# Optimization experiments

Hardware: AMD Instinct MI355X
Metric: run time of the kernel (lower is better)

The kernel has to match this reference:

```python
import jax, jax.numpy as jnp
import numpy as np

N, E, DIN, HID, HEADS = 50000, 400000, 256, 64, 4
EPS_BN = 1e-5

def setup_inputs() -> dict:
    key = jax.random.key(0)
    ks = jax.random.split(key, 12)
    inp = {}
    inp['x'] = jax.random.normal(ks[0], (N, DIN), dtype=jnp.float32)
    inp['edge_index'] = jax.random.randint(ks[1], (2, E), 0, N, dtype=jnp.int64)
    s = 1.0 / np.sqrt(DIN)
    inp['W1'] = jax.random.uniform(ks[2], (DIN, HEADS * HID), jnp.float32, -s, s)
    inp['a_src1'] = jax.random.normal(ks[3], (HEADS, HID), dtype=jnp.float32) * 0.1
    inp['a_dst1'] = jax.random.normal(ks[4], (HEADS, HID), dtype=jnp.float32) * 0.1
    inp['b1'] = jnp.zeros((HEADS * HID,), jnp.float32)
    inp['bn1_w'] = jnp.ones((HEADS * HID,), jnp.float32)
    inp['bn1_b'] = jnp.zeros((HEADS * HID,), jnp.float32)
    inp['bn1_m'] = jnp.zeros((HEADS * HID,), jnp.float32)
    inp['bn1_v'] = jnp.ones((HEADS * HID,), jnp.float32)
    s2 = 1.0 / np.sqrt(HEADS * HID)
    inp['W2'] = jax.random.uniform(ks[5], (HEADS * HID, HID), jnp.float32, -s2, s2)
    inp['a_src2'] = jax.random.normal(ks[6], (1, HID), dtype=jnp.float32) * 0.1
    inp['a_dst2'] = jax.random.normal(ks[7], (1, HID), dtype=jnp.float32) * 0.1
    inp['b2'] = jnp.zeros((HID,), jnp.float32)
    inp['bn2_w'] = jnp.ones((HID,), jnp.float32)
    inp['bn2_b'] = jnp.zeros((HID,), jnp.float32)
    inp['bn2_m'] = jnp.zeros((HID,), jnp.float32)
    inp['bn2_v'] = jnp.ones((HID,), jnp.float32)
    sr = 1.0 / np.sqrt(HID)
    inp['Wr'] = jax.random.uniform(ks[8], (HID, 1), jnp.float32, -sr, sr)
    inp['br'] = jnp.zeros((1,), jnp.float32)
    inp['Wc'] = jax.random.uniform(ks[9], (HID, 1), jnp.float32, -sr, sr)
    inp['bc'] = jnp.zeros((1,), jnp.float32)
    return inp

def gat_layer(x, src, dst, W, a_src, a_dst, bias, concat):
    # x: [N, Fin] -> h: [N, H, D]
    H, D = a_src.shape
    h = (x @ W).reshape(-1, H, D)
    alpha_s = jnp.sum(h * a_src[None], axis=-1)  # [N, H]
    alpha_d = jnp.sum(h * a_dst[None], axis=-1)
    e = jax.nn.leaky_relu(alpha_s[src] + alpha_d[dst], 0.2)  # [Et, H]
    m = jax.ops.segment_max(e, dst, num_segments=N)
    m = jnp.where(jnp.isfinite(m), m, 0.0)
    ex = jnp.exp(e - m[dst])
    denom = jax.ops.segment_sum(ex, dst, num_segments=N)
    alpha = ex / (denom[dst] + 1e-16)  # segment softmax over incoming edges
    msg = h[src] * alpha[:, :, None]  # [Et, H, D]
    out = jax.ops.segment_sum(msg, dst, num_segments=N)  # [N, H, D]
    out = out.reshape(N, H * D) if concat else out.mean(axis=1)
    return out + bias

def batchnorm(x, w, b, mean, var):
    return (x - mean) * jax.lax.rsqrt(var + EPS_BN) * w + b

def reference(x, edge_index, W1, a_src1, a_dst1, b1, bn1_w, bn1_b, bn1_m, bn1_v,
              W2, a_src2, a_dst2, b2, bn2_w, bn2_b, bn2_m, bn2_v, Wr, br, Wc, bc):
    # add self loops (PyG GATConv default)
    loops = jnp.arange(N, dtype=edge_index.dtype)
    src = jnp.concatenate([edge_index[0], loops])
    dst = jnp.concatenate([edge_index[1], loops])
    h = gat_layer(x, src, dst, W1, a_src1, a_dst1, b1, concat=True)
    h = jax.nn.elu(batchnorm(h, bn1_w, bn1_b, bn1_m, bn1_v))
    h = gat_layer(h, src, dst, W2, a_src2, a_dst2, b2, concat=False)
    h = jax.nn.elu(batchnorm(h, bn2_w, bn2_b, bn2_m, bn2_v))
    reg = h @ Wr + br
    clf = jax.nn.sigmoid(h @ Wc + bc)
    return reg, clf
```

## Files before the change

### kernel.cpp

```cpp
#include <hip/hip_runtime.h>
#include <math.h>


typedef unsigned short ushort_t;
typedef unsigned char uchar_t;
typedef __attribute__((ext_vector_type(8))) unsigned short ushort8;
typedef __attribute__((ext_vector_type(4))) unsigned short ushort4v;
typedef __attribute__((ext_vector_type(8))) short short8;
typedef __attribute__((ext_vector_type(4))) float f32x4;
typedef __attribute__((ext_vector_type(2))) float f32x2;

#define EPS_BN 1e-5f

__device__ __forceinline__ ushort_t f2bf(float f) {
  unsigned u = __float_as_uint(f);
  unsigned r = u + 0x7fffu + ((u >> 16) & 1u);
  return (ushort_t)(r >> 16);
}
__device__ __forceinline__ float bf2f(ushort_t h) {
  return __uint_as_float((unsigned)h << 16);
}
__device__ __forceinline__ uchar_t f2fp8(float f) {
  return (uchar_t)(__builtin_amdgcn_cvt_pk_fp8_f32(f, f, 0, false) & 0xff);
}
__device__ __forceinline__ float leaky02(float x) { return x >= 0.f ? x : 0.2f * x; }
__device__ __forceinline__ float elu_fast(float x) {
  return x > 0.f ? x : __expf(x) - 1.f;
}
__device__ __forceinline__ float wave_sum(float v) {
#pragma unroll
  for (int o = 1; o < 64; o <<= 1) v += __shfl_xor(v, o, 64);
  return v;
}
__device__ __forceinline__ int wave_incl_scan(int v, int lane) {
#pragma unroll
  for (int off = 1; off < 64; off <<= 1) {
    int t = __shfl_up(v, off, 64);
    if (lane >= off) v += t;
  }
  return v;
}

__device__ __forceinline__ void gld_lds16(const ushort_t* g, ushort_t* l) {
  __builtin_amdgcn_global_load_lds(
      (const __attribute__((address_space(1))) unsigned int*)g,
      (__attribute__((address_space(3))) unsigned int*)l, 16, 0, 0);
}

__global__ __launch_bounds__(256) void hist_kernel(
    const int* __restrict__ dst, int* __restrict__ counts, int E) {
  int e = blockIdx.x * blockDim.x + threadIdx.x;
  if (e < E) atomicAdd(&counts[dst[e]], 1);
}

__global__ __launch_bounds__(256) void scan_chunks_kernel(
    const int* __restrict__ counts, int* __restrict__ offsets, int* __restrict__ partials,
    int N, int E, int* __restrict__ csr_src,
    const float* __restrict__ W1, const float* __restrict__ W2,
    ushort_t* __restrict__ W1t, ushort_t* __restrict__ W2t,
    const float* __restrict__ b1, const float* __restrict__ bn1w,
    const float* __restrict__ bn1b, const float* __restrict__ bn1m,
    const float* __restrict__ bn1v,
    const float* __restrict__ b2, const float* __restrict__ bn2w,
    const float* __restrict__ bn2b, const float* __restrict__ bn2m,
    const float* __restrict__ bn2v,
    float* __restrict__ S1, float* __restrict__ T1,
    float* __restrict__ S2, float* __restrict__ T2) {
  __shared__ int ws[4];
  const int tid = threadIdx.x, lane = tid & 63, wv = tid >> 6;
  const int i = blockIdx.x * 256 + tid;
  const int gsz = gridDim.x * 256;
  int v = (i < N) ? counts[i] : 0;
  int incl = wave_incl_scan(v, lane);
  if (lane == 63) ws[wv] = incl;
  __syncthreads();
  int wbase = 0;
  for (int k = 0; k < wv; ++k) wbase += ws[k];
  if (i < N) offsets[i] = wbase + incl - v;
  if (tid == 255) partials[blockIdx.x] = wbase + incl;

  for (int j = i; j < 256 * 256; j += gsz) {
    int k = j >> 8, n2 = j & 255;
    W1t[n2 * 256 + k] = f2bf(W1[j]);
  }
  for (int j = i; j < 256 * 64; j += gsz) {
    int k = j >> 6, n2 = j & 63;
    W2t[n2 * 256 + k] = f2bf(W2[j]);
  }
  if (i < 256) {
    float s = bn1w[i] * rsqrtf(bn1v[i] + EPS_BN);
    S1[i] = s;
    T1[i] = (b1[i] - bn1m[i]) * s + bn1b[i];
  } else if (i < 320) {
    int j = i - 256;
    float s = bn2w[j] * rsqrtf(bn2v[j] + EPS_BN);
    S2[j] = s;
    T2[j] = (b2[j] - bn2m[j]) * s + bn2b[j];
  } else if (i < 384) {
    csr_src[E + i - 320] = 0;
  }
}

__global__ __launch_bounds__(256) void scatter_kernel(
    const int* __restrict__ src, const int* __restrict__ dst,
    const int* __restrict__ offsets, const int* __restrict__ partials,
    int* __restrict__ cursor, int* __restrict__ csr_src,
    int* __restrict__ offs2, int E, int N, int nb) {
  __shared__ int pp[256];
  __shared__ int ws[4];
  __shared__ int tot;
  const int tid = threadIdx.x, lane = tid & 63, wv = tid >> 6;
  int v = (tid < nb) ? partials[tid] : 0;
  int incl = wave_incl_scan(v, lane);
  if (lane == 63) ws[wv] = incl;
  __syncthreads();
  int wbase = 0;
  for (int k = 0; k < wv; ++k) wbase += ws[k];
  pp[tid] = wbase + incl - v;
  if (tid == 255) tot = wbase + incl;
  __syncthreads();

  int idx = blockIdx.x * 256 + tid;
  if (idx < E) {
    int d = dst[idx];
    int p = atomicAdd(&cursor[d], 1);
    csr_src[offsets[d] + pp[d >> 8] + p] = src[idx];
  }
  if (idx <= N) {
    offs2[idx] = (idx < N) ? offsets[idx] + pp[idx >> 8] : tot;
  }
}

__global__ __launch_bounds__(512) void gemm1_persist(
    const float* __restrict__ X, const ushort_t* __restrict__ Bt,
    uchar_t* __restrict__ Cout, const float* __restrict__ avs,
    const float* __restrict__ avd,
    float* __restrict__ as_out, float* __restrict__ ad_out, int M, int ntiles) {
  __shared__ ushort_t Bs[256 * 256];
  __shared__ ushort_t As[32 * 256];
  const int t = threadIdx.x;
  const int w = t >> 6, l = t & 63;
  const int wr = w >> 2, wc = w & 3;

#pragma unroll
  for (int it = 0; it < 16; ++it) {
    int s = it * 512 + t;
    int i = s >> 5, sr = s & 31;
    int kb = sr >> 3, sl8 = sr & 7;
    int kc = (sl8 ^ (i & 7)) << 3;
    gld_lds16(Bt + (size_t)i * 256 + kb * 64 + kc, &Bs[s * 8]);
  }

  const int ar = t >> 4, k0a = (t & 15) * 16;
  int wd0, wd1;
  {
    int k = k0a;
    wd0 = ar * 256 + (k & ~63) + ((k & 63) ^ ((ar & 7) << 3));
    k = k0a + 8;
    wd1 = ar * 256 + (k & ~63) + ((k & 63) ^ ((ar & 7) << 3));
  }
  float4 fa0, fa1, fa2, fa3;
  {
    const float* src = X + (size_t)min(blockIdx.x * 32 + ar, M - 1) * 256 + k0a;
    fa0 = *(const float4*)(src);
    fa1 = *(const float4*)(src + 4);
    fa2 = *(const float4*)(src + 8);
    fa3 = *(const float4*)(src + 12);
  }

  const int fr = l & 15;
  const int kq = (l >> 4) << 3;
  const int fx = (fr & 7) << 3;
  const ushort_t* Ab = &As[(wr * 16 + fr) << 8];
  const ushort_t* Bb = &Bs[(wc * 64 + fr) << 8];

  float asw[4], adw[4];
#pragma unroll
  for (int j = 0; j < 4; ++j) {
    asw[j] = avs[wc * 64 + fr + j * 16];
    adw[j] = avd[wc * 64 + fr + j * 16];
  }

  for (int tile = blockIdx.x; tile < ntiles; tile += 256) {
    ushort8 u0, u1;
    u0[0] = f2bf(fa0.x); u0[1] = f2bf(fa0.y); u0[2] = f2bf(fa0.z); u0[3] = f2bf(fa0.w);
    u0[4] = f2bf(fa1.x); u0[5] = f2bf(fa1.y); u0[6] = f2bf(fa1.z); u0[7] = f2bf(fa1.w);
    u1[0] = f2bf(fa2.x); u1[1] = f2bf(fa2.y); u1[2] = f2bf(fa2.z); u1[3] = f2bf(fa2.w);
    u1[4] = f2bf(fa3.x); u1[5] = f2bf(fa3.y); u1[6] = f2bf(fa3.z); u1[7] = f2bf(fa3.w);
    __syncthreads();
    *(ushort8*)&As[wd0] = u0;
    *(ushort8*)&As[wd1] = u1;
    __syncthreads();

    {
      int nt_ = tile + 256;
      if (nt_ < ntiles) {
        const float* src = X + (size_t)min(nt_ * 32 + ar, M - 1) * 256 + k0a;
        fa0 = *(const float4*)(src);
        fa1 = *(const float4*)(src + 4);
        fa2 = *(const float4*)(src + 8);
        fa3 = *(const float4*)(src + 12);
      }
    }

    f32x4 acc[4];
#pragma unroll
    for (int j = 0; j < 4; ++j) acc[j] = (f32x4){0.f, 0.f, 0.f, 0.f};
#pragma unroll
    for (int k0 = 0; k0 < 256; k0 += 32) {
      const int kabs = k0 + kq;
      const int base = (kabs & ~63) + ((kabs & 63) ^ fx);
      short8 af = *(const short8*)&Ab[base];
#pragma unroll
      for (int j = 0; j < 4; ++j) {
        short8 bf8 = *(const short8*)&Bb[j * 4096 + base];
        acc[j] = __builtin_amdgcn_mfma_f32_16x16x32_bf16(af, bf8, acc[j], 0, 0, 0);
      }
    }

    const int rbase = tile * 32 + wr * 16 + (l >> 4) * 4;
#pragma unroll
    for (int j = 0; j < 4; ++j)
#pragma unroll
      for (int r4 = 0; r4 < 4; ++r4) {
        int row = rbase + r4;
        if (row < M)
          Cout[(size_t)row * 256 + wc * 64 + fr + j * 16] = f2fp8(acc[j][r4]);
      }

#pragma unroll
    for (int r4 = 0; r4 < 4; ++r4) {
      float s_ = acc[0][r4] * asw[0] + acc[1][r4] * asw[1] +
                 acc[2][r4] * asw[2] + acc[3][r4] * asw[3];
      float d_ = acc[0][r4] * adw[0] + acc[1][r4] * adw[1] +
                 acc[2][r4] * adw[2] + acc[3][r4] * adw[3];
#pragma unroll
      for (int o = 1; o < 16; o <<= 1) {
        s_ += __shfl_xor(s_, o, 64);
        d_ += __shfl_xor(d_, o, 64);
      }
      if ((l & 15) == 0) {
        int row = rbase + r4;
        if (row < M) {
          as_out[(size_t)row * 4 + wc] = s_;
          ad_out[(size_t)row * 4 + wc] = d_;
        }
      }
    }
  }
}

__global__ __launch_bounds__(256) void gemm2_fullk(
    const ushort_t* __restrict__ Ain, const ushort_t* __restrict__ Bt,
    ushort_t* __restrict__ Cout, const float* __restrict__ avs,
    const float* __restrict__ avd,
    float* __restrict__ as_out, float* __restrict__ ad_out, int M) {
  __shared__ ushort_t As[64 * 256];
  __shared__ ushort_t Bs[64 * 256];
  const int t = threadIdx.x;
  const int w = t >> 6, l = t & 63;
  const int m0 = blockIdx.x * 64;

  {
    const int slot = l & 7;
#pragma unroll
    for (int i = 0; i < 8; ++i) {
      const int r = w * 64 + i * 8 + (l >> 3);
      const int ir = r >> 2, kb = r & 3;
      const int kc = (slot ^ (ir & 7)) << 3;
      gld_lds16(Bt + (size_t)ir * 256 + kb * 64 + kc, &Bs[w * 4096 + i * 512]);
    }
#pragma unroll
    for (int i = 0; i < 8; ++i) {
      const int r = w * 64 + i * 8 + (l >> 3);
      const int ir = r >> 2, kb = r & 3;
      const int kc = (slot ^ (ir & 7)) << 3;
      const int arow = min(m0 + ir, M - 1);
      gld_lds16(Ain + (size_t)arow * 256 + kb * 64 + kc, &As[w * 4096 + i * 512]);
    }
  }
  asm volatile("s_waitcnt vmcnt(8)" ::: "memory");
  __builtin_amdgcn_s_barrier();
  asm volatile("s_waitcnt vmcnt(0)" ::: "memory");
  __builtin_amdgcn_sched_barrier(0);

  f32x4 acc[4];
#pragma unroll
  for (int j = 0; j < 4; ++j) acc[j] = (f32x4){0.f, 0.f, 0.f, 0.f};

  const int fr = l & 15;
  const int kq = (l >> 4) << 3;
  const int fx = (fr & 7) << 3;
  const ushort_t* Ab = &As[(w * 16 + fr) << 8];
  const ushort_t* Bb = &Bs[fr << 8];
#pragma unroll
  for (int k0 = 0; k0 < 256; k0 += 32) {
    const int kabs = k0 + kq;
    const int base = (kabs & ~63) + ((kabs & 63) ^ fx);
    short8 af = *(const short8*)&Ab[base];
#pragma unroll
    for (int j = 0; j < 4; ++j) {
      short8 bf8 = *(const short8*)&Bb[j * 4096 + base];
      acc[j] = __builtin_amdgcn_mfma_f32_16x16x32_bf16(af, bf8, acc[j], 0, 0, 0);
    }
  }

  const int rbase = m0 + w * 16 + (l >> 4) * 4;
#pragma unroll
  for (int j = 0; j < 4; ++j)
#pragma unroll
    for (int r4 = 0; r4 < 4; ++r4) {
      int row = rbase + r4;
      if (row < M)
        Cout[(size_t)row * 64 + fr + j * 16] = f2bf(acc[j][r4]);
    }

  float asw[4], adw[4];
#pragma unroll
  for (int j = 0; j < 4; ++j) {
    asw[j] = avs[fr + j * 16];
    adw[j] = avd[fr + j * 16];
  }
#pragma unroll
  for (int r4 = 0; r4 < 4; ++r4) {
    float s_ = acc[0][r4] * asw[0] + acc[1][r4] * asw[1] +
               acc[2][r4] * asw[2] + acc[3][r4] * asw[3];
    float d_ = acc[0][r4] * adw[0] + acc[1][r4] * adw[1] +
               acc[2][r4] * adw[2] + acc[3][r4] * adw[3];
#pragma unroll
    for (int o = 1; o < 16; o <<= 1) {
      s_ += __shfl_xor(s_, o, 64);
      d_ += __shfl_xor(d_, o, 64);
    }
    if ((l & 15) == 0) {
      int row = rbase + r4;
      if (row < M) {
        as_out[row] = s_;
        ad_out[row] = d_;
      }
    }
  }
}

__global__ __launch_bounds__(256) void agg1_kernel(
    const uchar_t* __restrict__ h1, const int* __restrict__ offsets,
    const int* __restrict__ csr, const float* __restrict__ as1,
    const float* __restrict__ ad1,
    const float* __restrict__ S1, const float* __restrict__ T1,
    ushort_t* __restrict__ out, int N) {
  __shared__ float ldsW[4][64][4];
  const int wv = threadIdx.x >> 6;
  int n = blockIdx.x * 4 + wv;
  int l = threadIdx.x & 63;
  if (n >= N) return;
  const int hh = l >> 4;
  int off = offsets[n], deg = offsets[n + 1] - off;
  const int* csrp = csr + off;
  const unsigned fb = (unsigned)l << 2;
  float4 adn = *(const float4*)&ad1[n * 4];
  float ad_h = (hh & 2) ? ((hh & 1) ? adn.w : adn.z) : ((hh & 1) ? adn.y : adn.x);

  f32x2 acc0 = {0.f, 0.f}, acc1 = {0.f, 0.f};
  float den = 0.f;

  for (int base = 0; base < deg; base += 64) {
    int cnt = min(64, deg - base);
    int s = 0;
    float4 w4 = make_float4(0.f, 0.f, 0.f, 0.f);
    if (l < cnt) {
      s = csrp[base + l];
      float4 a4 = *(const float4*)&as1[s * 4];
      w4.x = __expf(leaky02(a4.x + adn.x));
      w4.y = __expf(leaky02(a4.y + adn.y));
      w4.z = __expf(leaky02(a4.z + adn.z));
      w4.w = __expf(leaky02(a4.w + adn.w));
    }
    *(float4*)&ldsW[wv][l][0] = w4;
    for (int j = 0; j < cnt; j += 8) {
#pragma unroll
      for (int i = 0; i < 8; ++i) {
        int e = j + i;
        unsigned se = (unsigned)__builtin_amdgcn_readlane(s, e);
        float we = ldsW[wv][e][hh];
        unsigned q = *(const unsigned*)(h1 + (size_t)((se << 8) + fb));
        f32x2 lo = __builtin_amdgcn_cvt_pk_f32_fp8(q, false);
        f32x2 hi = __builtin_amdgcn_cvt_pk_f32_fp8(q, true);
        f32x2 w2 = {we, we};
        acc0 = lo * w2 + acc0;
        acc1 = hi * w2 + acc1;
        den += we;
      }
    }
  }

  float4 asn = *(const float4*)&as1[n * 4];
  float as_h = (hh & 2) ? ((hh & 1) ? asn.w : asn.z) : ((hh & 1) ? asn.y : asn.x);
  float ws = __expf(leaky02(as_h + ad_h));
  {
    unsigned q = *(const unsigned*)(h1 + (size_t)(((unsigned)n << 8) + fb));
    f32x2 lo = __builtin_amdgcn_cvt_pk_f32_fp8(q, false);
    f32x2 hi = __builtin_amdgcn_cvt_pk_f32_fp8(q, true);
    f32x2 w2 = {ws, ws};
    acc0 = lo * w2 + acc0;
    acc1 = hi * w2 + acc1;
  }
  float inv = 1.f / (den + ws + 1e-16f);

  const int c0 = l * 4;
  float4 Sv = *(const float4*)&S1[c0];
  float4 Tv = *(const float4*)&T1[c0];
  float o0 = fmaf(acc0.x, inv * Sv.x, Tv.x);
  float o1 = fmaf(acc0.y, inv * Sv.y, Tv.y);
  float o2 = fmaf(acc1.x, inv * Sv.z, Tv.z);
  float o3 = fmaf(acc1.y, inv * Sv.w, Tv.w);
  ushort4v o4;
  o4[0] = f2bf(elu_fast(o0));
  o4[1] = f2bf(elu_fast(o1));
  o4[2] = f2bf(elu_fast(o2));
  o4[3] = f2bf(elu_fast(o3));
  *(ushort4v*)&out[(size_t)n * 256 + c0] = o4;
}

__global__ __launch_bounds__(256) void agg2_kernel(
    const ushort_t* __restrict__ h2, const int* __restrict__ offsets,
    const int* __restrict__ csr, const float* __restrict__ as2,
    const float* __restrict__ ad2,
    const float* __restrict__ S2, const float* __restrict__ T2,
    const float* __restrict__ Wr, const float* __restrict__ br,
    const float* __restrict__ Wc, const float* __restrict__ bc,
    float* __restrict__ out_reg, float* __restrict__ out_clf, int N) {
  __shared__ float2 ldsSW[4][64];
  const int wv = threadIdx.x >> 6;
  const int l = threadIdx.x & 63;
  const int h = l >> 5, q = l & 31;
  int n = blockIdx.x * 8 + wv * 2 + h;
  const bool valid = (n < N);
  if (!valid) n = N - 1;
  const int off = offsets[n], deg = offsets[n + 1] - off;
  const int* csrp = csr + off;
  const float adn = ad2[n];
  const int degw = max(deg, __shfl_xor(deg, 32, 64));

  f32x2 acc = {0.f, 0.f};
  float den = 0.f;
  const int hb = h << 5;

  for (int base = 0; base < degw; base += 32) {
    int s = 0;
    float w_ = 0.f;
    int idx = base + q;
    if (idx < deg) {
      s = csrp[idx];
      w_ = __expf(leaky02(as2[s] + adn));
    }
    float2 sw;
    sw.x = __int_as_float(s);
    sw.y = w_;
    ldsSW[wv][l] = sw;
    int cntw = min(32, degw - base);
    for (int j = 0; j < cntw; j += 8) {
#pragma unroll
      for (int i = 0; i < 8; ++i) {
        int e = j + i;
        float2 t = ldsSW[wv][hb + e];
        int se = __float_as_int(t.x);
        float we = t.y;
        unsigned d = *(const unsigned*)&h2[(size_t)se * 64 + (q << 1)];
        acc.x = fmaf(we, bf2f((ushort_t)d), acc.x);
        acc.y = fmaf(we, bf2f((ushort_t)(d >> 16)), acc.y);
        den += we;
      }
    }
  }

  float ws = __expf(leaky02(as2[n] + adn));
  {
    unsigned d = *(const unsigned*)&h2[(size_t)n * 64 + (q << 1)];
    acc.x = fmaf(ws, bf2f((ushort_t)d), acc.x);
    acc.y = fmaf(ws, bf2f((ushort_t)(d >> 16)), acc.y);
  }
  float inv = 1.f / (den + ws + 1e-16f);

  const int c0 = q << 1;
  float2 Sv = *(const float2*)&S2[c0];
  float2 Tv = *(const float2*)&T2[c0];
  float2 wr = *(const float2*)&Wr[c0];
  float2 wc = *(const float2*)&Wc[c0];
  float o0 = elu_fast(fmaf(acc.x, inv * Sv.x, Tv.x));
  float o1 = elu_fast(fmaf(acc.y, inv * Sv.y, Tv.y));
  float rs = o0 * wr.x + o1 * wr.y;
  float cs = o0 * wc.x + o1 * wc.y;
#pragma unroll
  for (int o = 1; o < 32; o <<= 1) {
    rs += __shfl_xor(rs, o, 64);
    cs += __shfl_xor(cs, o, 64);
  }
  if (q == 0 && valid) {
    out_reg[n] = rs + br[0];
    float z = cs + bc[0];
    out_clf[n] = 1.f / (1.f + __expf(-z));
  }
}

extern "C" void kernel_launch(void* const* d_in, const int* in_sizes, int n_in,
                              void* d_out, int out_size, void* d_ws, size_t ws_size,
                              hipStream_t stream) {
  const float* x      = (const float*)d_in[0];
  const int*   ei     = (const int*)d_in[1];
  const float* W1     = (const float*)d_in[2];
  const float* a_src1 = (const float*)d_in[3];
  const float* a_dst1 = (const float*)d_in[4];
  const float* b1     = (const float*)d_in[5];
  const float* bn1w   = (const float*)d_in[6];
  const float* bn1b   = (const float*)d_in[7];
  const float* bn1m   = (const float*)d_in[8];
  const float* bn1v   = (const float*)d_in[9];
  const float* W2     = (const float*)d_in[10];
  const float* a_src2 = (const float*)d_in[11];
  const float* a_dst2 = (const float*)d_in[12];
  const float* b2     = (const float*)d_in[13];
  const float* bn2w   = (const float*)d_in[14];
  const float* bn2b   = (const float*)d_in[15];
  const float* bn2m   = (const float*)d_in[16];
  const float* bn2v   = (const float*)d_in[17];
  const float* Wr     = (const float*)d_in[18];
  const float* br     = (const float*)d_in[19];
  const float* Wc     = (const float*)d_in[20];
  const float* bc     = (const float*)d_in[21];

  const int N = in_sizes[0] / 256;
  const int E = in_sizes[1] / 2;
  const int* srcv = ei;
  const int* dstv = ei + E;

  char* w = (char*)d_ws;
  auto alloc = [&](size_t bytes) {
    char* p = w;
    w += (bytes + 255) & ~(size_t)255;
    return p;
  };
  const int nb = (N + 255) / 256;
  const size_t nbytes_rounded = ((size_t)N * 4 + 255) & ~(size_t)255;
  int* counts    = (int*)alloc((size_t)N * 4);
  int* cursor    = (int*)alloc((size_t)N * 4);
  int* offsets   = (int*)alloc((size_t)N * 4);
  int* offs2     = (int*)alloc((size_t)(N + 1) * 4);
  int* partials  = (int*)alloc((size_t)nb * 4);
  int* csr_src   = (int*)alloc((size_t)(E + 64) * 4);
  float* as1     = (float*)alloc((size_t)N * 4 * 4);
  float* ad1     = (float*)alloc((size_t)N * 4 * 4);
  float* as2     = (float*)alloc((size_t)N * 4);
  float* ad2     = (float*)alloc((size_t)N * 4);
  float* S1      = (float*)alloc(256 * 4);
  float* T1      = (float*)alloc(256 * 4);
  float* S2      = (float*)alloc(64 * 4);
  float* T2      = (float*)alloc(64 * 4);
  ushort_t* W1t  = (ushort_t*)alloc((size_t)256 * 256 * 2);
  ushort_t* W2t  = (ushort_t*)alloc((size_t)64 * 256 * 2);
  uchar_t* h1b   = (uchar_t*)alloc((size_t)N * 256);
  ushort_t* h1a  = (ushort_t*)alloc((size_t)N * 256 * 2);
  ushort_t* h2b  = (ushort_t*)alloc((size_t)N * 64 * 2);

  float* out_reg = (float*)d_out;

  hipMemsetAsync(counts, 0, nbytes_rounded * 2, stream);
  hist_kernel<<<(E + 255) / 256, 256, 0, stream>>>(dstv, counts, E);
  scan_chunks_kernel<<<nb, 256, 0, stream>>>(counts, offsets, partials, N, E, csr_src,
                                             W1, W2, W1t, W2t,
                                             b1, bn1w, bn1b, bn1m, bn1v,
                                             b2, bn2w, bn2b, bn2m, bn2v,
                                             S1, T1, S2, T2);
  {
    int items = max(E, N + 1);
    scatter_kernel<<<(items + 255) / 256, 256, 0, stream>>>(srcv, dstv, offsets, partials,
                                                            cursor, csr_src, offs2, E, N, nb);
  }

  const int nwb = (N + 3) / 4;
  const int nwb2 = (N + 7) / 8;
  const int ntiles1 = (N + 31) / 32;
  const int mtiles2 = (N + 63) / 64;

  gemm1_persist<<<256, 512, 0, stream>>>(
      x, W1t, h1b, a_src1, a_dst1, as1, ad1, N, ntiles1);
  agg1_kernel<<<nwb, 256, 0, stream>>>(h1b, offs2, csr_src, as1, ad1, S1, T1, h1a, N);

  gemm2_fullk<<<mtiles2, 256, 0, stream>>>(
      h1a, W2t, h2b, a_src2, a_dst2, as2, ad2, N);
  agg2_kernel<<<nwb2, 256, 0, stream>>>(h2b, offs2, csr_src, as2, ad2, S2, T2,
                                        Wr, br, Wc, bc, out_reg, out_reg + N, N);
}
```

Before: 242.1 us.

## Process two nodes per wavefront in layer-1 aggregation with 8-byte gathers

The layer-1 aggregation kernel now maps two destination nodes onto each 64-lane wavefront, one per half-wave. Each lane gathers 8 fp8 features per neighbour with a uint2 load instead of 4. Source indices are shared through LDS rather than readlane, and the grid is halved to 8 nodes per block. The aim is to use lanes better on the many low-degree nodes and issue wider loads. The cost is that each pair of nodes loops to the larger of their two degrees, so some lanes sit idle.

```diff
diff --git a/kernel.cpp b/kernel.cpp
--- a/kernel.cpp
+++ b/kernel.cpp
@@ -348,77 +348,94 @@
     const float* __restrict__ ad1,
     const float* __restrict__ S1, const float* __restrict__ T1,
     ushort_t* __restrict__ out, int N) {
+  __shared__ int ldsS[4][64];
   __shared__ float ldsW[4][64][4];
   const int wv = threadIdx.x >> 6;
-  int n = blockIdx.x * 4 + wv;
-  int l = threadIdx.x & 63;
-  if (n >= N) return;
-  const int hh = l >> 4;
-  int off = offsets[n], deg = offsets[n + 1] - off;
+  const int l = threadIdx.x & 63;
+  const int h = l >> 5, q = l & 31;
+  const int hb = h << 5;
+  const int hh = q >> 3;
+  int n = blockIdx.x * 8 + wv * 2 + h;
+  const bool valid = (n < N);
+  if (!valid) n = N - 1;
+  const int off = offsets[n], deg = offsets[n + 1] - off;
   const int* csrp = csr + off;
-  const unsigned fb = (unsigned)l << 2;
+  const unsigned fb = (unsigned)q << 3;
   float4 adn = *(const float4*)&ad1[n * 4];
-  float ad_h = (hh & 2) ? ((hh & 1) ? adn.w : adn.z) : ((hh & 1) ? adn.y : adn.x);
-
-  f32x2 acc0 = {0.f, 0.f}, acc1 = {0.f, 0.f};
+  const int degw = max(deg, __shfl_xor(deg, 32, 64));
+
+  f32x2 a0 = {0.f, 0.f}, a1 = {0.f, 0.f}, a2 = {0.f, 0.f}, a3 = {0.f, 0.f};
   float den = 0.f;
 
-  for (int base = 0; base < deg; base += 64) {
-    int cnt = min(64, deg - base);
+  for (int base = 0; base < degw; base += 32) {
     int s = 0;
     float4 w4 = make_float4(0.f, 0.f, 0.f, 0.f);
-    if (l < cnt) {
-      s = csrp[base + l];
+    int idx = base + q;
+    if (idx < deg) {
+      s = csrp[idx];
       float4 a4 = *(const float4*)&as1[s * 4];
       w4.x = __expf(leaky02(a4.x + adn.x));
       w4.y = __expf(leaky02(a4.y + adn.y));
       w4.z = __expf(leaky02(a4.z + adn.z));
       w4.w = __expf(leaky02(a4.w + adn.w));
     }
+    ldsS[wv][l] = s;
     *(float4*)&ldsW[wv][l][0] = w4;
-    for (int j = 0; j < cnt; j += 8) {
+    int cntw = min(32, degw - base);
+    for (int j = 0; j < cntw; j += 8) {
 #pragma unroll
       for (int i = 0; i < 8; ++i) {
         int e = j + i;
-        unsigned se = (unsigned)__builtin_amdgcn_readlane(s, e);
-        float we = ldsW[wv][e][hh];
-        unsigned q = *(const unsigned*)(h1 + (size_t)((se << 8) + fb));
-        f32x2 lo = __builtin_amdgcn_cvt_pk_f32_fp8(q, false);
-        f32x2 hi = __builtin_amdgcn_cvt_pk_f32_fp8(q, true);
+        int se = ldsS[wv][hb + e];
+        float we = ldsW[wv][hb + e][hh];
+        uint2 d = *(const uint2*)&h1[(size_t)se * 256 + fb];
+        f32x2 lo0 = __builtin_amdgcn_cvt_pk_f32_fp8(d.x, false);
+        f32x2 hi0 = __builtin_amdgcn_cvt_pk_f32_fp8(d.x, true);
+        f32x2 lo1 = __builtin_amdgcn_cvt_pk_f32_fp8(d.y, false);
+        f32x2 hi1 = __builtin_amdgcn_cvt_pk_f32_fp8(d.y, true);
         f32x2 w2 = {we, we};
-        acc0 = lo * w2 + acc0;
-        acc1 = hi * w2 + acc1;
+        a0 = lo0 * w2 + a0;
+        a1 = hi0 * w2 + a1;
+        a2 = lo1 * w2 + a2;
+        a3 = hi1 * w2 + a3;
         den += we;
       }
     }
   }
 
+  float ad_h = (hh & 2) ? ((hh & 1) ? adn.w : adn.z) : ((hh & 1) ? adn.y : adn.x);
   float4 asn = *(const float4*)&as1[n * 4];
   float as_h = (hh & 2) ? ((hh & 1) ? asn.w : asn.z) : ((hh & 1) ? asn.y : asn.x);
   float ws = __expf(leaky02(as_h + ad_h));
   {
-    unsigned q = *(const unsigned*)(h1 + (size_t)(((unsigned)n << 8) + fb));
-    f32x2 lo = __builtin_amdgcn_cvt_pk_f32_fp8(q, false);
-    f32x2 hi = __builtin_amdgcn_cvt_pk_f32_fp8(q, true);
+    uint2 d = *(const uint2*)&h1[(size_t)n * 256 + fb];
+    f32x2 lo0 = __builtin_amdgcn_cvt_pk_f32_fp8(d.x, false);
+    f32x2 hi0 = __builtin_amdgcn_cvt_pk_f32_fp8(d.x, true);
+    f32x2 lo1 = __builtin_amdgcn_cvt_pk_f32_fp8(d.y, false);
+    f32x2 hi1 = __builtin_amdgcn_cvt_pk_f32_fp8(d.y, true);
     f32x2 w2 = {ws, ws};
-    acc0 = lo * w2 + acc0;
-    acc1 = hi * w2 + acc1;
+    a0 = lo0 * w2 + a0;
+    a1 = hi0 * w2 + a1;
+    a2 = lo1 * w2 + a2;
+    a3 = hi1 * w2 + a3;
   }
   float inv = 1.f / (den + ws + 1e-16f);
 
-  const int c0 = l * 4;
-  float4 Sv = *(const float4*)&S1[c0];
-  float4 Tv = *(const float4*)&T1[c0];
-  float o0 = fmaf(acc0.x, inv * Sv.x, Tv.x);
-  float o1 = fmaf(acc0.y, inv * Sv.y, Tv.y);
-  float o2 = fmaf(acc1.x, inv * Sv.z, Tv.z);
-  float o3 = fmaf(acc1.y, inv * Sv.w, Tv.w);
-  ushort4v o4;
-  o4[0] = f2bf(elu_fast(o0));
-  o4[1] = f2bf(elu_fast(o1));
-  o4[2] = f2bf(elu_fast(o2));
-  o4[3] = f2bf(elu_fast(o3));
-  *(ushort4v*)&out[(size_t)n * 256 + c0] = o4;
+  const int c0 = q << 3;
+  float4 Sv0 = *(const float4*)&S1[c0];
+  float4 Sv1 = *(const float4*)&S1[c0 + 4];
+  float4 Tv0 = *(const float4*)&T1[c0];
+  float4 Tv1 = *(const float4*)&T1[c0 + 4];
+  ushort8 o;
+  o[0] = f2bf(elu_fast(fmaf(a0.x, inv * Sv0.x, Tv0.x)));
+  o[1] = f2bf(elu_fast(fmaf(a0.y, inv * Sv0.y, Tv0.y)));
+  o[2] = f2bf(elu_fast(fmaf(a1.x, inv * Sv0.z, Tv0.z)));
+  o[3] = f2bf(elu_fast(fmaf(a1.y, inv * Sv0.w, Tv0.w)));
+  o[4] = f2bf(elu_fast(fmaf(a2.x, inv * Sv1.x, Tv1.x)));
+  o[5] = f2bf(elu_fast(fmaf(a2.y, inv * Sv1.y, Tv1.y)));
+  o[6] = f2bf(elu_fast(fmaf(a3.x, inv * Sv1.z, Tv1.z)));
+  o[7] = f2bf(elu_fast(fmaf(a3.y, inv * Sv1.w, Tv1.w)));
+  if (valid) *(ushort8*)&out[(size_t)n * 256 + c0] = o;
 }
 
 __global__ __launch_bounds__(256) void agg2_kernel(
@@ -576,17 +593,16 @@
                                                             cursor, csr_src, offs2, E, N, nb);
   }
 
-  const int nwb = (N + 3) / 4;
-  const int nwb2 = (N + 7) / 8;
+  const int nwb8 = (N + 7) / 8;
   const int ntiles1 = (N + 31) / 32;
   const int mtiles2 = (N + 63) / 64;
 
   gemm1_persist<<<256, 512, 0, stream>>>(
       x, W1t, h1b, a_src1, a_dst1, as1, ad1, N, ntiles1);
-  agg1_kernel<<<nwb, 256, 0, stream>>>(h1b, offs2, csr_src, as1, ad1, S1, T1, h1a, N);
+  agg1_kernel<<<nwb8, 256, 0, stream>>>(h1b, offs2, csr_src, as1, ad1, S1, T1, h1a, N);
 
   gemm2_fullk<<<mtiles2, 256, 0, stream>>>(
       h1a, W2t, h2b, a_src2, a_dst2, as2, ad2, N);
-  agg2_kernel<<<nwb2, 256, 0, stream>>>(h2b, offs2, csr_src, as2, ad2, S2, T2,
+  agg2_kernel<<<nwb8, 256, 0, stream>>>(h2b, offs2, csr_src, as2, ad2, S2, T2,
                                         Wr, br, Wc, bc, out_reg, out_reg + N, N);
 }
```

Result: no change. 243.9 us (+0.7%).
